# Performance work log

Measured on AMD Instinct MI355X. Metric: run time of the kernel, lower is better.

The kernel has to match this reference:

```python
import jax, jax.numpy as jnp
import numpy as np
from jax import lax

B, T_ENC, T_DEC = 64, 512, 500
MEL, PRE, ENC_D, H, ATT = 80, 256, 512, 1024, 128


def conv1d(x, w, b, pad):
    # x: [B,Cin,T], w: [Cout,Cin,K]
    y = lax.conv_general_dilated(x, w, (1,), [(pad, pad)], dimension_numbers=('NCH', 'OIH', 'NCH'))
    return y + b[None, :, None]


def lstm_cell(x, h, c, w_ih, w_hh, b_ih, b_hh):
    # PyTorch gate order: i, f, g, o
    g = x @ w_ih.T + h @ w_hh.T + b_ih + b_hh
    i, f, gg, o = jnp.split(g, 4, axis=-1)
    c2 = jax.nn.sigmoid(f) * c + jax.nn.sigmoid(i) * jnp.tanh(gg)
    return jax.nn.sigmoid(o) * jnp.tanh(c2), c2


def setup_inputs() -> dict:
    key = jax.random.key(0)
    ks = iter(jax.random.split(key, 64))
    def rn(*shape):
        return jax.random.normal(next(ks), shape, jnp.float32) * 0.05
    return dict(
        enc=jax.random.normal(next(ks), (B, T_ENC, ENC_D), jnp.float32),
        mel_tgt=jax.random.normal(next(ks), (B, T_DEC, MEL), jnp.float32),
        p1w=rn(PRE, MEL), p1b=rn(PRE), p2w=rn(PRE, PRE), p2b=rn(PRE),
        wih0=rn(4 * H, PRE + ENC_D), whh0=rn(4 * H, H), bih0=rn(4 * H), bhh0=rn(4 * H),
        wih1=rn(4 * H, H), whh1=rn(4 * H, H), bih1=rn(4 * H), bhh1=rn(4 * H),
        aq=rn(ATT, H), am=rn(ATT, ENC_D), al=rn(ATT, 32),
        alcw=rn(32, 1, 31), alcb=rn(32), ae=rn(1, ATT), ab=jnp.zeros((ATT,), jnp.float32),
        mw=rn(MEL, H + ENC_D), mb=rn(MEL), sw=rn(1, H + ENC_D), sb=rn(1),
        pw0=rn(512, MEL, 5), pb0=rn(512), bg0=jnp.ones((512,), jnp.float32), bb0=rn(512),
        pw1=rn(512, 512, 5), pb1=rn(512), bg1=jnp.ones((512,), jnp.float32), bb1=rn(512),
        pw2=rn(512, 512, 5), pb2=rn(512), bg2=jnp.ones((512,), jnp.float32), bb2=rn(512),
        pw3=rn(512, 512, 5), pb3=rn(512), bg3=jnp.ones((512,), jnp.float32), bb3=rn(512),
        pw4=rn(MEL, 512, 5), pb4=rn(MEL), bg4=jnp.ones((MEL,), jnp.float32), bb4=rn(MEL),
    )


def reference(enc, mel_tgt, p1w, p1b, p2w, p2b,
              wih0, whh0, bih0, bhh0, wih1, whh1, bih1, bhh1,
              aq, am, al, alcw, alcb, ae, ab, mw, mb, sw, sb,
              pw0, pb0, bg0, bb0, pw1, pb1, bg1, bb1, pw2, pb2, bg2, bb2,
              pw3, pb3, bg3, bb3, pw4, pb4, bg4, bb4):
    Bz, Te, _ = enc.shape
    mem = enc @ am.T  # [B,Te,128] (memory projection hoisted out of the loop)
    # teacher forcing: prev_mel at t=0 is zeros, then mel_tgt[:, t-1]
    prev = jnp.concatenate([jnp.zeros((Bz, 1, MEL), enc.dtype), mel_tgt[:, :-1]], axis=1)
    xs = jnp.swapaxes(prev, 0, 1)  # [Td,B,80]
    init = (jnp.zeros((Bz, Te), enc.dtype),
            jnp.zeros((2, Bz, H), enc.dtype),
            jnp.zeros((2, Bz, H), enc.dtype))

    def step(carry, pm):
        att_prev, h, c = carry
        # prenet (eval mode: dropout disabled)
        pre = jax.nn.relu(jax.nn.relu(pm @ p1w.T + p1b) @ p2w.T + p2b)  # [B,256]
        # location-sensitive attention
        loc = conv1d(att_prev[:, None, :], alcw, alcb, 15)  # [B,32,Te]
        loc = jnp.swapaxes(loc, 1, 2) @ al.T                # [B,Te,128]
        q = (h[1] @ aq.T)[:, None, :]                       # [B,1,128]
        e = jnp.tanh(q + mem + loc + ab) @ ae.T             # [B,Te,1]
        att = jax.nn.softmax(e[..., 0], axis=1)             # [B,Te]
        ctx = jnp.einsum('bt,btd->bd', att, enc)            # [B,512]
        # 2-layer LSTM on single step
        h0, c0 = lstm_cell(jnp.concatenate([pre, ctx], -1), h[0], c[0], wih0, whh0, bih0, bhh0)
        h1, c1 = lstm_cell(h0, h[1], c[1], wih1, whh1, bih1, bhh1)
        pi = jnp.concatenate([h1, ctx], -1)                 # [B,1536]
        mel = pi @ mw.T + mb                                # [B,80]
        stop = pi @ sw.T + sb                               # [B,1]
        return (att, jnp.stack([h0, h1]), jnp.stack([c0, c1])), (mel, stop, att)

    _, (mels, stops, atts) = lax.scan(step, init, xs)
    mel = jnp.swapaxes(mels, 0, 1)    # [B,Td,80]
    stop = jnp.swapaxes(stops, 0, 1)  # [B,Td,1]
    attw = jnp.swapaxes(atts, 0, 1)   # [B,Td,Te]
    # postnet (BatchNorm1d in eval mode: running_mean=0, running_var=1)
    eps = 1e-5
    def bn(x, g, bt):
        return x * (g / jnp.sqrt(1.0 + eps))[None, :, None] + bt[None, :, None]
    x = jnp.swapaxes(mel, 1, 2)  # [B,80,Td]
    x = jnp.tanh(bn(conv1d(x, pw0, pb0, 2), bg0, bb0))
    x = jnp.tanh(bn(conv1d(x, pw1, pb1, 2), bg1, bb1))
    x = jnp.tanh(bn(conv1d(x, pw2, pb2, 2), bg2, bb2))
    x = jnp.tanh(bn(conv1d(x, pw3, pb3, 2), bg3, bb3))
    x = bn(conv1d(x, pw4, pb4, 2), bg4, bb4)
    post = jnp.swapaxes(x, 1, 2)
    return mel + post, mel, stop, attw
```

## Files before the change

### kernel.cpp

```cpp
#include <hip/hip_runtime.h>
#include <math.h>


static constexpr long OFF_AMT  = 0;
static constexpr long OFF_P1WT = OFF_AMT  + 512L*128;
static constexpr long OFF_P2WT = OFF_P1WT + 80L*256;
static constexpr long OFF_MWT  = OFF_P2WT + 256L*256;
static constexpr long OFF_AQT  = OFF_MWT  + 1536L*80;
static constexpr long OFF_WLOC = OFF_AQT  + 1024L*128;
static constexpr long OFF_BLOC = OFF_WLOC + 128L*32;
static constexpr long OFF_WLT  = OFF_BLOC + 128;
static constexpr long OFF_GB0  = OFF_WLT  + 4096;
static constexpr long OFF_GB1  = OFF_GB0  + 4096;
static constexpr long OFF_PWT0 = OFF_GB1  + 4096;
static constexpr long OFF_PWT1 = OFF_PWT0 + 400L*512;
static constexpr long OFF_PWT2 = OFF_PWT1 + 2560L*512;
static constexpr long OFF_PWT3 = OFF_PWT2 + 2560L*512;
static constexpr long OFF_PWT4 = OFF_PWT3 + 2560L*512;
static constexpr long OFF_PRE  = OFF_PWT4 + 2560L*80;
static constexpr long OFF_MEM  = OFF_PRE  + 500L*64*256;
static constexpr long OFF_H0A  = OFF_MEM  + 64L*512*128;
static constexpr long OFF_H0B  = OFF_H0A  + 64L*1024;
static constexpr long OFF_H1A  = OFF_H0B  + 64L*1024;
static constexpr long OFF_H1B  = OFF_H1A  + 64L*1024;
static constexpr long OFF_C0   = OFF_H1B  + 64L*1024;
static constexpr long OFF_C1   = OFF_C0   + 64L*1024;
static constexpr long OFF_Q    = OFF_C1   + 64L*1024;
static constexpr long OFF_CTX  = OFF_Q    + 64L*128;
static constexpr long OFF_EBUF = OFF_CTX  + 64L*512;
static constexpr long OFF_PB0  = OFF_EBUF + 64L*512;
static constexpr long OFF_PB1  = OFF_PB0  + 64L*512*500;
static constexpr long WS_FLOATS = OFF_PB1 + 64L*512*500;

static constexpr long OFF_BAR = OFF_PB0;

static constexpr long DO_MEL  = 64L*500*80;
static constexpr long DO_STOP = 2*DO_MEL;
static constexpr long DO_ATT  = DO_STOP + 64L*500;

static constexpr long ZERO_CNT = OFF_EBUF - OFF_H0A;
static constexpr long PREP_TOTAL = ZERO_CNT + 4096 + 4096 + 4096 + 128 + 4096
  + 65536 + 20480 + 65536 + 122880 + 131072
  + 204800 + 1310720 + 1310720 + 1310720 + 204800;

static constexpr int NBLK = 256;
static constexpr int NTHR = 512;

typedef float f4 __attribute__((ext_vector_type(4)));

__device__ __forceinline__ float fsigmoid(float x) { return 1.f / (1.f + __expf(-x)); }
__device__ __forceinline__ float ftanh(float x) {
  float ax = fminf(fabsf(x), 15.f);
  float e = __expf(-2.f * ax);
  float r = (1.f - e) / (1.f + e);
  return copysignf(r, x);
}
__device__ __forceinline__ float4 ld4(const float* p) { return *(const float4*)p; }
__device__ __forceinline__ f4 ld4v(const float* p) { return *(const f4*)p; }
__device__ __forceinline__ float dot4(float4 w, float4 x, float acc) {
  acc = fmaf(w.x, x.x, acc); acc = fmaf(w.y, x.y, acc);
  acc = fmaf(w.z, x.z, acc); acc = fmaf(w.w, x.w, acc);
  return acc;
}
__device__ __forceinline__ float dot4v(f4 w, float4 x, float acc) {
  acc = fmaf(w.x, x.x, acc); acc = fmaf(w.y, x.y, acc);
  acc = fmaf(w.z, x.z, acc); acc = fmaf(w.w, x.w, acc);
  return acc;
}

__device__ __forceinline__ void gbar(unsigned* bar, unsigned gen) {
  __syncthreads();
  if (blockIdx.x == 0) {
    if (threadIdx.x > 0 && threadIdx.x < 256) {
      while (__hip_atomic_load(&bar[threadIdx.x*16], __ATOMIC_RELAXED,
                               __HIP_MEMORY_SCOPE_AGENT) != gen)
        __builtin_amdgcn_s_sleep(1);
    }
    __syncthreads();
    if (threadIdx.x == 0)
      __hip_atomic_store(&bar[4096], gen, __ATOMIC_RELEASE, __HIP_MEMORY_SCOPE_AGENT);
  } else {
    if (threadIdx.x == 0) {
      __hip_atomic_store(&bar[blockIdx.x*16], gen, __ATOMIC_RELEASE,
                         __HIP_MEMORY_SCOPE_AGENT);
      while (__hip_atomic_load(&bar[4096], __ATOMIC_RELAXED,
                               __HIP_MEMORY_SCOPE_AGENT) != gen)
        __builtin_amdgcn_s_sleep(1);
    }
  }
  if (threadIdx.x == 0) __threadfence();
  __syncthreads();
}

__global__ __launch_bounds__(256) void k_prep(
    const float* __restrict__ bih0, const float* __restrict__ bhh0,
    const float* __restrict__ bih1, const float* __restrict__ bhh1,
    const float* __restrict__ al,   const float* __restrict__ alcw,
    const float* __restrict__ alcb, const float* __restrict__ ab,
    const float* __restrict__ am,   const float* __restrict__ p1w,
    const float* __restrict__ p2w,  const float* __restrict__ mw,
    const float* __restrict__ aq,
    const float* __restrict__ pw0, const float* __restrict__ pw1,
    const float* __restrict__ pw2, const float* __restrict__ pw3,
    const float* __restrict__ pw4,
    float* __restrict__ ws)
{
  if (blockIdx.x == 0) {
    unsigned* bar = (unsigned*)(ws + OFF_BAR);
    for (int i = threadIdx.x; i < 4160; i += 256) bar[i] = 0u;
  }
  long stride = (long)gridDim.x * 256;
  for (long idx = (long)blockIdx.x * 256 + threadIdx.x; idx < PREP_TOTAL; idx += stride) {
    long r = idx;
    if (r < ZERO_CNT) { ws[OFF_H0A + r] = 0.f; continue; }
    r -= ZERO_CNT;
    if (r < 4096) { ws[OFF_GB0 + r] = bih0[r] + bhh0[r]; continue; }
    r -= 4096;
    if (r < 4096) { ws[OFF_GB1 + r] = bih1[r] + bhh1[r]; continue; }
    r -= 4096;
    if (r < 4096) {
      int a = (int)(r >> 5), k = (int)(r & 31);
      float v = 0.f;
      if (k < 31) for (int ch = 0; ch < 32; ++ch) v += al[a*32 + ch] * alcw[ch*31 + k];
      ws[OFF_WLOC + r] = v; continue;
    }
    r -= 4096;
    if (r < 128) {
      float v = ab[r];
      for (int ch = 0; ch < 32; ++ch) v += al[r*32 + ch] * alcb[ch];
      ws[OFF_BLOC + r] = v; continue;
    }
    r -= 128;
    if (r < 4096) {
      int k = (int)(r >> 7), a = (int)(r & 127);
      float v = 0.f;
      if (k < 31) for (int ch = 0; ch < 32; ++ch) v += al[a*32 + ch] * alcw[ch*31 + k];
      ws[OFF_WLT + r] = v; continue;
    }
    r -= 4096;
    if (r < 65536) { int d = (int)(r >> 7), a2 = (int)(r & 127); ws[OFF_AMT + r] = am[(long)a2*512 + d]; continue; }
    r -= 65536;
    if (r < 20480) { int k = (int)(r >> 8), j = (int)(r & 255); ws[OFF_P1WT + r] = p1w[j*80 + k]; continue; }
    r -= 20480;
    if (r < 65536) { int k = (int)(r >> 8), j = (int)(r & 255); ws[OFF_P2WT + r] = p2w[j*256 + k]; continue; }
    r -= 65536;
    if (r < 122880) { int k = (int)(r / 80), c = (int)(r % 80); ws[OFF_MWT + r] = mw[(long)c*1536 + k]; continue; }
    r -= 122880;
    if (r < 131072) { int k = (int)(r >> 7), a2 = (int)(r & 127); ws[OFF_AQT + r] = aq[(long)a2*1024 + k]; continue; }
    r -= 131072;
    if (r < 204800) { int c5 = (int)(r / 512), co = (int)(r % 512); ws[OFF_PWT0 + r] = pw0[((long)co*80  + c5/5)*5 + (c5%5)]; continue; }
    r -= 204800;
    if (r < 1310720) { int c5 = (int)(r / 512), co = (int)(r % 512); ws[OFF_PWT1 + r] = pw1[((long)co*512 + c5/5)*5 + (c5%5)]; continue; }
    r -= 1310720;
    if (r < 1310720) { int c5 = (int)(r / 512), co = (int)(r % 512); ws[OFF_PWT2 + r] = pw2[((long)co*512 + c5/5)*5 + (c5%5)]; continue; }
    r -= 1310720;
    if (r < 1310720) { int c5 = (int)(r / 512), co = (int)(r % 512); ws[OFF_PWT3 + r] = pw3[((long)co*512 + c5/5)*5 + (c5%5)]; continue; }
    r -= 1310720;
    { int c5 = (int)(r / 80), co = (int)(r % 80); ws[OFF_PWT4 + r] = pw4[((long)co*512 + c5/5)*5 + (c5%5)]; }
  }
}

__global__ __launch_bounds__(256) void k_prenet(
    const float* __restrict__ mel_tgt, const float* __restrict__ p1b,
    const float* __restrict__ p2b, float* __restrict__ ws)
{
  int t = blockIdx.x, tid = threadIdx.x;
  const float* p1wT = ws + OFF_P1WT;
  const float* p2wT = ws + OFF_P2WT;
  __shared__ float prev_s[16][80];
  __shared__ float h1_s[16][256];
  for (int sb = 0; sb < 4; ++sb) {
    int b0 = sb * 16;
    for (int i = tid; i < 16*80; i += 256) {
      int rr = i / 80, k = i - rr*80;
      float v = 0.f;
      if (t > 0) v = mel_tgt[((long)(b0 + rr)*500 + (t-1))*80 + k];
      prev_s[rr][k] = v;
    }
    __syncthreads();
    int j = tid;
    for (int rr = 0; rr < 16; ++rr) {
      float acc = p1b[j];
      for (int k = 0; k < 80; ++k) acc = fmaf(prev_s[rr][k], p1wT[k*256 + j], acc);
      h1_s[rr][j] = fmaxf(acc, 0.f);
    }
    __syncthreads();
    for (int rr = 0; rr < 16; ++rr) {
      float acc = p2b[j];
      for (int k = 0; k < 256; ++k) acc = fmaf(h1_s[rr][k], p2wT[k*256 + j], acc);
      ws[OFF_PRE + ((long)t*64 + b0 + rr)*256 + j] = fmaxf(acc, 0.f);
    }
    __syncthreads();
  }
}

__global__ __launch_bounds__(256) void k_mem(const float* __restrict__ enc, float* __restrict__ ws)
{
  int row0 = blockIdx.x * 16;
  int tid = threadIdx.x;
  int a = tid & 127, rh = tid >> 7;
  const float* amT = ws + OFF_AMT;
  __shared__ float encS[16][65];
  float acc[8];
#pragma unroll
  for (int i = 0; i < 8; ++i) acc[i] = 0.f;
  for (int k0 = 0; k0 < 512; k0 += 64) {
    for (int i = tid; i < 16*64; i += 256) {
      int rr = i >> 6, kk = i & 63;
      encS[rr][kk] = enc[(long)(row0 + rr)*512 + k0 + kk];
    }
    __syncthreads();
    for (int kk = 0; kk < 64; ++kk) {
      float w = amT[(long)(k0 + kk)*128 + a];
#pragma unroll
      for (int rr = 0; rr < 8; ++rr) acc[rr] = fmaf(encS[rh*8 + rr][kk], w, acc[rr]);
    }
    __syncthreads();
  }
#pragma unroll
  for (int rr = 0; rr < 8; ++rr)
    ws[OFF_MEM + (long)(row0 + rh*8 + rr)*128 + a] = acc[rr];
}

struct SmemE { float ap[160]; float bq[128]; float ep[4][132]; };
struct SmemS { float es[512]; float wred[8]; float wsum[8]; float red[16][132]; };
struct SmemG { float xw[8][8][64]; float gsh[16][65]; };
struct SmemM { float xs[1536]; };
union SmemU { SmemE e; SmemS s; SmemG g; SmemM m; };

__global__ __launch_bounds__(NTHR, 2) void k_decode(
    const float* __restrict__ enc, const float* __restrict__ ae,
    const float* __restrict__ wih0, const float* __restrict__ whh0,
    const float* __restrict__ wih1, const float* __restrict__ whh1,
    const float* __restrict__ mw, const float* __restrict__ mb,
    const float* __restrict__ sw, const float* __restrict__ sb,
    const float* __restrict__ aq,
    float* __restrict__ dout, float* __restrict__ ws)
{
  const int B = blockIdx.x;
  const int tid = threadIdx.x;
  unsigned* bar = (unsigned*)(ws + OFF_BAR);
  unsigned gen = 0;

  __shared__ float WlTs[4096];
  __shared__ float aeS[128];
  __shared__ SmemU U;

  for (int i = tid; i < 4096; i += NTHR) WlTs[i] = ws[OFF_WLT + i];
  if (tid < 128) aeS[tid] = ae[tid];
  __syncthreads();

  for (int t = 0; t < 500; ++t) {
    const int p = t & 1;

    {
      const int b = B & 63, cc2 = B >> 6;
      const int te0 = cc2 * 128;
      const int tel = tid & 127, ag = tid >> 7;
      const int a0 = ag * 32;
      for (int i = tid; i < 158; i += NTHR) {
        int gte = te0 + i - 15;
        float v = 0.f;
        if (t > 0 && gte >= 0 && gte < 512)
          v = dout[DO_ATT + ((long)b*500 + (t-1))*512 + gte];
        U.e.ap[i] = v;
      }
      if (tid < 128) U.e.bq[tid] = ws[OFF_Q + b*128 + tid] + ws[OFF_BLOC + tid];
      __syncthreads();
      float acc[32];
#pragma unroll
      for (int i = 0; i < 32; ++i) acc[i] = 0.f;
      for (int k = 0; k < 31; ++k) {
        float apk = U.e.ap[tel + k];
#pragma unroll
        for (int a4 = 0; a4 < 8; ++a4) {
          float4 wv = ld4(&WlTs[k*128 + a0 + a4*4]);
          acc[a4*4+0] = fmaf(apk, wv.x, acc[a4*4+0]);
          acc[a4*4+1] = fmaf(apk, wv.y, acc[a4*4+1]);
          acc[a4*4+2] = fmaf(apk, wv.z, acc[a4*4+2]);
          acc[a4*4+3] = fmaf(apk, wv.w, acc[a4*4+3]);
        }
      }
      const float* memp = ws + OFF_MEM + ((long)b*512 + te0 + tel)*128 + a0;
      float esum = 0.f;
#pragma unroll
      for (int a4 = 0; a4 < 8; ++a4) {
        f4 mv = ld4v(&memp[a4*4]);
        float4 bq = ld4(&U.e.bq[a0 + a4*4]);
        float4 av = ld4(&aeS[a0 + a4*4]);
        esum = fmaf(av.x, ftanh(acc[a4*4+0] + bq.x + mv.x), esum);
        esum = fmaf(av.y, ftanh(acc[a4*4+1] + bq.y + mv.y), esum);
        esum = fmaf(av.z, ftanh(acc[a4*4+2] + bq.z + mv.z), esum);
        esum = fmaf(av.w, ftanh(acc[a4*4+3] + bq.w + mv.w), esum);
      }
      U.e.ep[ag][tel] = esum;
      __syncthreads();
      if (tid < 128)
        ws[OFF_EBUF + (long)b*512 + te0 + tid] =
            U.e.ep[0][tid] + U.e.ep[1][tid] + U.e.ep[2][tid] + U.e.ep[3][tid];
    }
    gbar(bar, ++gen);

    {
      const int b = B & 63, q4 = B >> 6;
      const float* eb = ws + OFF_EBUF + (long)b*512;
      float v = eb[tid];
      float m = v;
#pragma unroll
      for (int o = 32; o; o >>= 1) m = fmaxf(m, __shfl_xor(m, o));
      if ((tid & 63) == 0) U.s.wred[tid >> 6] = m;
      __syncthreads();
      float mx = U.s.wred[0];
#pragma unroll
      for (int i2 = 1; i2 < 8; ++i2) mx = fmaxf(mx, U.s.wred[i2]);
      float pe = __expf(v - mx);
      U.s.es[tid] = pe;
      float s = pe;
#pragma unroll
      for (int o = 32; o; o >>= 1) s += __shfl_xor(s, o);
      if ((tid & 63) == 0) U.s.wsum[tid >> 6] = s;
      __syncthreads();
      float tot = U.s.wsum[0];
#pragma unroll
      for (int i2 = 1; i2 < 8; ++i2) tot += U.s.wsum[i2];
      float inv = 1.f / tot;
      if (tid < 128)
        dout[DO_ATT + ((long)b*500 + t)*512 + q4*128 + tid] = U.s.es[q4*128 + tid] * inv;
      const int dq = tid & 31, th = tid >> 5;
      const float* ep = enc + (long)b*262144 + q4*128 + dq*4;
      float4 a4 = {0.f, 0.f, 0.f, 0.f};
#pragma unroll 8
      for (int te = th*32; te < th*32 + 32; ++te) {
        float sc = U.s.es[te];
        f4 ev = ld4v(&ep[(long)te*512]);
        a4.x = fmaf(sc, ev.x, a4.x); a4.y = fmaf(sc, ev.y, a4.y);
        a4.z = fmaf(sc, ev.z, a4.z); a4.w = fmaf(sc, ev.w, a4.w);
      }
      *(float4*)&U.s.red[th][dq*4] = a4;
      __syncthreads();
      if (tid < 128) {
        float sm = 0.f;
#pragma unroll
        for (int th2 = 0; th2 < 16; ++th2) sm += U.s.red[th2][tid];
        ws[OFF_CTX + (long)b*512 + q4*128 + tid] = sm * inv;
      }
    }
    gbar(bar, ++gen);

#pragma unroll 1
    for (int mode = 0; mode < 2; ++mode) {
      const int l = tid & 63, w = tid >> 6;
      const int jr = l & 15, kq = l >> 4;
      const int bs8 = w * 8;
      const long j = (long)(jr >> 2)*1024 + B*4 + (jr & 3);
      const int KH = mode ? 1024 : 768;
      const int LD = mode ? 1024 : 768;
      const int NC = mode ? 32 : 28;
      const float* wih = mode ? wih1 : wih0;
      const float* whh = mode ? whh1 : whh0;
      const float* gbp = ws + (mode ? OFF_GB1 : OFF_GB0);
      const float* srcPre = ws + OFF_PRE + (long)t*64*256;
      const float* srcCtx = ws + OFF_CTX;
      const float* h0r = ws + OFF_H0A + (long)p*65536;
      const float* h0n = ws + OFF_H0A + (long)(1-p)*65536;
      const float* h1r = ws + OFF_H1A + (long)p*65536;
      float* xw = &U.g.xw[w][0][0];

      const int bx0 = l >> 4, kx0 = (l & 15) * 4;

      auto xsrc = [&](int bx, int k) -> float4 {
        const int gb_ = bs8 + bx;
        if (mode == 0) {
          if (k < 256)  return ld4(srcPre + gb_*256 + k);
          if (k < 768)  return ld4(srcCtx + gb_*512 + (k - 256));
          return ld4(h0r + gb_*1024 + (k - 768));
        }
        return (k < 1024) ? ld4(h0n + gb_*1024 + k) : ld4(h1r + gb_*1024 + (k - 1024));
      };

      f4 wr0, wr1, wr2, wr3, wn0, wn1, wn2, wn3;
      float4 xA, xB;
      {
        const int bk = kq * 16;
        const float* wp = (bk < KH) ? (wih + j*LD + bk) : (whh + j*1024 + (bk - KH));
        wr0 = ld4v(wp); wr1 = ld4v(wp + 4); wr2 = ld4v(wp + 8); wr3 = ld4v(wp + 12);
        xA = xsrc(bx0, kx0);
        xB = xsrc(4 + bx0, kx0);
      }
      float acc[8];
#pragma unroll
      for (int i = 0; i < 8; ++i) acc[i] = 0.f;

      for (int c = 0; c < NC; ++c) {
        *(float4*)(xw + l*4)       = xA;
        *(float4*)(xw + 256 + l*4) = xB;
        if (c + 1 < NC) {
          const int bk = (c+1)*64 + kq*16;
          const float* wp = (bk < KH) ? (wih + j*LD + bk) : (whh + j*1024 + (bk - KH));
          wn0 = ld4v(wp); wn1 = ld4v(wp + 4); wn2 = ld4v(wp + 8); wn3 = ld4v(wp + 12);
          xA = xsrc(bx0, (c+1)*64 + kx0);
          xB = xsrc(4 + bx0, (c+1)*64 + kx0);
        }
        asm volatile("s_waitcnt lgkmcnt(0)" ::: "memory");
        __builtin_amdgcn_sched_barrier(0);
#pragma unroll
        for (int i = 0; i < 8; ++i) {
          const float* xp = xw + i*64 + kq*16;
          float4 x0 = ld4(xp), x1 = ld4(xp + 4), x2 = ld4(xp + 8), x3 = ld4(xp + 12);
          acc[i] = dot4v(wr3, x3, dot4v(wr2, x2, dot4v(wr1, x1, dot4v(wr0, x0, acc[i]))));
        }
        __builtin_amdgcn_sched_barrier(0);
        wr0 = wn0; wr1 = wn1; wr2 = wn2; wr3 = wn3;
      }

#pragma unroll
      for (int i = 0; i < 8; ++i) {
        acc[i] += __shfl_xor(acc[i], 16);
        acc[i] += __shfl_xor(acc[i], 32);
      }
      if (kq == 0) {
        float bias = gbp[j];
#pragma unroll
        for (int i = 0; i < 8; ++i) U.g.gsh[jr][bs8 + i] = acc[i] + bias;
      }
      __syncthreads();
      if (tid < 256) {
        const int b2 = tid & 63, u4 = tid >> 6;
        float iv = U.g.gsh[u4][b2];
        float fv = U.g.gsh[4 + u4][b2];
        float gv = U.g.gsh[8 + u4][b2];
        float ov = U.g.gsh[12 + u4][b2];
        long hw = (mode ? OFF_H1A : OFF_H0A) + (long)(1-p)*65536 + (long)b2*1024 + B*4 + u4;
        long cw = (mode ? OFF_C1 : OFF_C0) + (long)b2*1024 + B*4 + u4;
        float cold = ws[cw];
        float c2 = fsigmoid(fv)*cold + fsigmoid(iv)*ftanh(gv);
        ws[cw] = c2;
        ws[hw] = fsigmoid(ov)*ftanh(c2);
      }
      gbar(bar, ++gen);
    }

    {
      const int b = B & 63, part = B >> 6;
      const float* h1n = ws + OFF_H1A + (long)(1-p)*65536;
      const float* ctx = ws + OFF_CTX;
      for (int i = tid; i < 1536; i += NTHR)
        U.m.xs[i] = (i < 1024) ? h1n[b*1024 + i] : ctx[b*512 + (i - 1024)];
      __syncthreads();
      const int grp = tid >> 3, l8 = tid & 7;
      const int kb = l8 * 4;
      if (part == 0 || (part == 3 && grp < 16)) {
        const int jj = (part == 0) ? grp : 64 + grp;
        const float* wrp = mw + (long)jj*1536;
        float4 a4 = {0.f, 0.f, 0.f, 0.f};
#pragma unroll 8
        for (int i = 0; i < 48; ++i) {
          float4 xv = ld4(&U.m.xs[kb + i*32]);
          float4 wv = ld4(&wrp[kb + i*32]);
          a4.x = fmaf(xv.x, wv.x, a4.x); a4.y = fmaf(xv.y, wv.y, a4.y);
          a4.z = fmaf(xv.z, wv.z, a4.z); a4.w = fmaf(xv.w, wv.w, a4.w);
        }
        float acc = (a4.x + a4.y) + (a4.z + a4.w);
        acc += __shfl_xor(acc, 1);
        acc += __shfl_xor(acc, 2);
        acc += __shfl_xor(acc, 4);
        if (l8 == 0) dout[DO_MEL + ((long)b*500 + t)*80 + jj] = acc + mb[jj];
      } else if (part == 1 || part == 2) {
        const int a = (part - 1)*64 + grp;
        const float* wrp = aq + (long)a*1024;
        float4 a4 = {0.f, 0.f, 0.f, 0.f};
#pragma unroll 8
        for (int i = 0; i < 32; ++i) {
          float4 xv = ld4(&U.m.xs[kb + i*32]);
          float4 wv = ld4(&wrp[kb + i*32]);
          a4.x = fmaf(xv.x, wv.x, a4.x); a4.y = fmaf(xv.y, wv.y, a4.y);
          a4.z = fmaf(xv.z, wv.z, a4.z); a4.w = fmaf(xv.w, wv.w, a4.w);
        }
        float acc = (a4.x + a4.y) + (a4.z + a4.w);
        acc += __shfl_xor(acc, 1);
        acc += __shfl_xor(acc, 2);
        acc += __shfl_xor(acc, 4);
        if (l8 == 0) ws[OFF_Q + b*128 + a] = acc;
      } else if (part == 3 && grp == 16) {
        float4 a4 = {0.f, 0.f, 0.f, 0.f};
#pragma unroll 8
        for (int i = 0; i < 48; ++i) {
          float4 xv = ld4(&U.m.xs[kb + i*32]);
          float4 wv = ld4(&sw[kb + i*32]);
          a4.x = fmaf(xv.x, wv.x, a4.x); a4.y = fmaf(xv.y, wv.y, a4.y);
          a4.z = fmaf(xv.z, wv.z, a4.z); a4.w = fmaf(xv.w, wv.w, a4.w);
        }
        float acc = (a4.x + a4.y) + (a4.z + a4.w);
        acc += __shfl_xor(acc, 1);
        acc += __shfl_xor(acc, 2);
        acc += __shfl_xor(acc, 4);
        if (l8 == 0) dout[DO_STOP + (long)b*500 + t] = acc + sb[0];
      }
    }
    gbar(bar, ++gen);
  }
}

__global__ __launch_bounds__(256) void k_conv(
    const float* __restrict__ in, float* __restrict__ out,
    const float* __restrict__ wT, const float* __restrict__ pb,
    const float* __restrict__ bg, const float* __restrict__ bbp,
    const float* __restrict__ melp,
    int CI, int CO, int flags)
{
  int tx = blockIdx.x, cy = blockIdx.y, b = blockIdx.z;
  int tid = threadIdx.x;
  int tl = tid & 63;
  int cog = __builtin_amdgcn_readfirstlane((int)(tid >> 6));
  int t0 = tx * 64;
  int co0 = cy*64 + cog*16;
  __shared__ float xs[16][68];
  float acc[16];
#pragma unroll
  for (int i = 0; i < 16; ++i) acc[i] = 0.f;
  for (int ci0 = 0; ci0 < CI; ci0 += 16) {
    for (int i = tid; i < 16*68; i += 256) {
      int cl = i / 68, tt = i - cl*68;
      int tg = t0 + tt - 2;
      float v = 0.f;
      if (tg >= 0 && tg < 500) {
        if (flags & 1) v = in[((long)b*500 + tg)*80 + (ci0 + cl)];
        else           v = in[((long)b*CI + ci0 + cl)*500 + tg];
      }
      xs[cl][tt] = v;
    }
    __syncthreads();
    for (int cl = 0; cl < 16; ++cl) {
#pragma unroll
      for (int k = 0; k < 5; ++k) {
        const float* wr = wT + ((long)((ci0 + cl)*5 + k))*CO + co0;
        float xv = xs[cl][tl + k];
#pragma unroll
        for (int i = 0; i < 16; ++i) acc[i] = fmaf(xv, wr[i], acc[i]);
      }
    }
    __syncthreads();
  }
  int tg = t0 + tl;
  if (tg < 500) {
    const float RS = 0.99999500003749969f;
#pragma unroll
    for (int i = 0; i < 16; ++i) {
      int co = co0 + i;
      if (co < CO) {
        float sc = bg[co] * RS;
        float v = fmaf(acc[i], sc, fmaf(pb[co], sc, bbp[co]));
        if (flags & 4) v = ftanh(v);
        if (flags & 2) { long oi = ((long)b*500 + tg)*80 + co; out[oi] = melp[oi] + v; }
        else out[((long)b*CO + co)*500 + tg] = v;
      }
    }
  }
}

extern "C" void kernel_launch(void* const* d_in, const int* in_sizes, int n_in,
                              void* d_out, int out_size, void* d_ws, size_t ws_size,
                              hipStream_t stream)
{
  (void)in_sizes; (void)n_in; (void)out_size; (void)ws_size;
  const float* enc     = (const float*)d_in[0];
  const float* mel_tgt = (const float*)d_in[1];
  const float* p1w = (const float*)d_in[2];
  const float* p1b = (const float*)d_in[3];
  const float* p2w = (const float*)d_in[4];
  const float* p2b = (const float*)d_in[5];
  const float* wih0 = (const float*)d_in[6];
  const float* whh0 = (const float*)d_in[7];
  const float* bih0 = (const float*)d_in[8];
  const float* bhh0 = (const float*)d_in[9];
  const float* wih1 = (const float*)d_in[10];
  const float* whh1 = (const float*)d_in[11];
  const float* bih1 = (const float*)d_in[12];
  const float* bhh1 = (const float*)d_in[13];
  const float* aq   = (const float*)d_in[14];
  const float* am   = (const float*)d_in[15];
  const float* al   = (const float*)d_in[16];
  const float* alcw = (const float*)d_in[17];
  const float* alcb = (const float*)d_in[18];
  const float* ae   = (const float*)d_in[19];
  const float* ab   = (const float*)d_in[20];
  const float* mw   = (const float*)d_in[21];
  const float* mb   = (const float*)d_in[22];
  const float* sw   = (const float*)d_in[23];
  const float* sb   = (const float*)d_in[24];
  const float* pw0 = (const float*)d_in[25];
  const float* pb0 = (const float*)d_in[26];
  const float* bg0 = (const float*)d_in[27];
  const float* bb0 = (const float*)d_in[28];
  const float* pw1 = (const float*)d_in[29];
  const float* pb1 = (const float*)d_in[30];
  const float* bg1 = (const float*)d_in[31];
  const float* bb1 = (const float*)d_in[32];
  const float* pw2 = (const float*)d_in[33];
  const float* pb2 = (const float*)d_in[34];
  const float* bg2 = (const float*)d_in[35];
  const float* bb2 = (const float*)d_in[36];
  const float* pw3 = (const float*)d_in[37];
  const float* pb3 = (const float*)d_in[38];
  const float* bg3 = (const float*)d_in[39];
  const float* bb3 = (const float*)d_in[40];
  const float* pw4 = (const float*)d_in[41];
  const float* pb4 = (const float*)d_in[42];
  const float* bg4 = (const float*)d_in[43];
  const float* bb4 = (const float*)d_in[44];

  float* ws = (float*)d_ws;
  float* dout = (float*)d_out;

  k_prep<<<dim3(2048), 256, 0, stream>>>(bih0, bhh0, bih1, bhh1, al, alcw, alcb, ab,
                                         am, p1w, p2w, mw, aq, pw0, pw1, pw2, pw3, pw4, ws);
  k_prenet<<<dim3(500), 256, 0, stream>>>(mel_tgt, p1b, p2b, ws);
  k_mem<<<dim3(2048), 256, 0, stream>>>(enc, ws);

  k_decode<<<dim3(NBLK), NTHR, 0, stream>>>(enc, ae, wih0, whh0, wih1, whh1,
                                            mw, mb, sw, sb, aq, dout, ws);

  k_conv<<<dim3(8, 8, 64), 256, 0, stream>>>(dout + DO_MEL, ws + OFF_PB0, ws + OFF_PWT0,
                                             pb0, bg0, bb0, nullptr, 80, 512, 1 | 4);
  k_conv<<<dim3(8, 8, 64), 256, 0, stream>>>(ws + OFF_PB0, ws + OFF_PB1, ws + OFF_PWT1,
                                             pb1, bg1, bb1, nullptr, 512, 512, 4);
  k_conv<<<dim3(8, 8, 64), 256, 0, stream>>>(ws + OFF_PB1, ws + OFF_PB0, ws + OFF_PWT2,
                                             pb2, bg2, bb2, nullptr, 512, 512, 4);
  k_conv<<<dim3(8, 8, 64), 256, 0, stream>>>(ws + OFF_PB0, ws + OFF_PB1, ws + OFF_PWT3,
                                             pb3, bg3, bb3, nullptr, 512, 512, 4);
  k_conv<<<dim3(8, 2, 64), 256, 0, stream>>>(ws + OFF_PB1, dout, ws + OFF_PWT4,
                                             pb4, bg4, bb4, dout + DO_MEL, 512, 80, 2);
}
```

Before: 95.20 ms.

## Double persistent decode grid to 512 blocks and repartition all per-step phases

The persistent decoder grows from 256 to 512 blocks at 4 blocks per CU. Each block now handles half as much work: 64 encoder positions for the attention energies, 64 context columns, and 2 hidden units per LSTM gate instead of 4, with an extra shuffle stage for the smaller K slices. The grid barrier is extended so block 0 polls 512 arrival flags, and the output-projection phase is reassigned so only the first 256 blocks work. The goal is more parallelism and latency hiding in the weight-streaming GEMV phases, at the cost of a wider barrier and more per-block overhead.

```diff
diff --git a/kernel.cpp b/kernel.cpp
--- a/kernel.cpp
+++ b/kernel.cpp
@@ -43,7 +43,7 @@
   + 65536 + 20480 + 65536 + 122880 + 131072
   + 204800 + 1310720 + 1310720 + 1310720 + 204800;
 
-static constexpr int NBLK = 256;
+static constexpr int NBLK = 512;
 static constexpr int NTHR = 512;
 
 typedef float f4 __attribute__((ext_vector_type(4)));
@@ -57,11 +57,6 @@
 }
 __device__ __forceinline__ float4 ld4(const float* p) { return *(const float4*)p; }
 __device__ __forceinline__ f4 ld4v(const float* p) { return *(const f4*)p; }
-__device__ __forceinline__ float dot4(float4 w, float4 x, float acc) {
-  acc = fmaf(w.x, x.x, acc); acc = fmaf(w.y, x.y, acc);
-  acc = fmaf(w.z, x.z, acc); acc = fmaf(w.w, x.w, acc);
-  return acc;
-}
 __device__ __forceinline__ float dot4v(f4 w, float4 x, float acc) {
   acc = fmaf(w.x, x.x, acc); acc = fmaf(w.y, x.y, acc);
   acc = fmaf(w.z, x.z, acc); acc = fmaf(w.w, x.w, acc);
@@ -71,19 +66,27 @@
 __device__ __forceinline__ void gbar(unsigned* bar, unsigned gen) {
   __syncthreads();
   if (blockIdx.x == 0) {
-    if (threadIdx.x > 0 && threadIdx.x < 256) {
-      while (__hip_atomic_load(&bar[threadIdx.x*16], __ATOMIC_RELAXED,
+    const int t = threadIdx.x;
+    if (t > 0 && t < 256) {
+      while (__hip_atomic_load(&bar[t*16], __ATOMIC_RELAXED,
                                __HIP_MEMORY_SCOPE_AGENT) != gen)
         __builtin_amdgcn_s_sleep(1);
-    }
-    __syncthreads();
-    if (threadIdx.x == 0)
-      __hip_atomic_store(&bar[4096], gen, __ATOMIC_RELEASE, __HIP_MEMORY_SCOPE_AGENT);
+      while (__hip_atomic_load(&bar[(t + 256)*16], __ATOMIC_RELAXED,
+                               __HIP_MEMORY_SCOPE_AGENT) != gen)
+        __builtin_amdgcn_s_sleep(1);
+    } else if (t == 0) {
+      while (__hip_atomic_load(&bar[256*16], __ATOMIC_RELAXED,
+                               __HIP_MEMORY_SCOPE_AGENT) != gen)
+        __builtin_amdgcn_s_sleep(1);
+    }
+    __syncthreads();
+    if (t == 0)
+      __hip_atomic_store(&bar[8192], gen, __ATOMIC_RELEASE, __HIP_MEMORY_SCOPE_AGENT);
   } else {
     if (threadIdx.x == 0) {
       __hip_atomic_store(&bar[blockIdx.x*16], gen, __ATOMIC_RELEASE,
                          __HIP_MEMORY_SCOPE_AGENT);
-      while (__hip_atomic_load(&bar[4096], __ATOMIC_RELAXED,
+      while (__hip_atomic_load(&bar[8192], __ATOMIC_RELAXED,
                                __HIP_MEMORY_SCOPE_AGENT) != gen)
         __builtin_amdgcn_s_sleep(1);
     }
@@ -107,7 +110,7 @@
 {
   if (blockIdx.x == 0) {
     unsigned* bar = (unsigned*)(ws + OFF_BAR);
-    for (int i = threadIdx.x; i < 4160; i += 256) bar[i] = 0u;
+    for (int i = threadIdx.x; i < 8320; i += 256) bar[i] = 0u;
   }
   long stride = (long)gridDim.x * 256;
   for (long idx = (long)blockIdx.x * 256 + threadIdx.x; idx < PREP_TOTAL; idx += stride) {
@@ -222,13 +225,13 @@
     ws[OFF_MEM + (long)(row0 + rh*8 + rr)*128 + a] = acc[rr];
 }
 
-struct SmemE { float ap[160]; float bq[128]; float ep[4][132]; };
-struct SmemS { float es[512]; float wred[8]; float wsum[8]; float red[16][132]; };
-struct SmemG { float xw[8][8][64]; float gsh[16][65]; };
+struct SmemE { float ap[94]; float bq[128]; float ep[8][68]; };
+struct SmemS { float es[512]; float wred[8]; float wsum[8]; float red[32][68]; };
+struct SmemG { float xw[8][8][64]; float gsh[8][65]; };
 struct SmemM { float xs[1536]; };
 union SmemU { SmemE e; SmemS s; SmemG g; SmemM m; };
 
-__global__ __launch_bounds__(NTHR, 2) void k_decode(
+__global__ __launch_bounds__(NTHR, 4) void k_decode(
     const float* __restrict__ enc, const float* __restrict__ ae,
     const float* __restrict__ wih0, const float* __restrict__ whh0,
     const float* __restrict__ wih1, const float* __restrict__ whh1,
@@ -254,26 +257,27 @@
     const int p = t & 1;
 
     {
-      const int b = B & 63, cc2 = B >> 6;
-      const int te0 = cc2 * 128;
-      const int tel = tid & 127, ag = tid >> 7;
-      const int a0 = ag * 32;
-      for (int i = tid; i < 158; i += NTHR) {
-        int gte = te0 + i - 15;
+      const int b = B & 63, cc = B >> 6;
+      const int te0 = cc * 64;
+      const int tel = tid & 63, ag = tid >> 6;
+      const int a0 = ag * 16;
+      if (tid < 94) {
+        int gte = te0 + tid - 15;
         float v = 0.f;
         if (t > 0 && gte >= 0 && gte < 512)
           v = dout[DO_ATT + ((long)b*500 + (t-1))*512 + gte];
-        U.e.ap[i] = v;
-      }
-      if (tid < 128) U.e.bq[tid] = ws[OFF_Q + b*128 + tid] + ws[OFF_BLOC + tid];
+        U.e.ap[tid] = v;
+      }
+      if (tid >= 128 && tid < 256)
+        U.e.bq[tid - 128] = ws[OFF_Q + b*128 + (tid - 128)] + ws[OFF_BLOC + (tid - 128)];
       __syncthreads();
-      float acc[32];
-#pragma unroll
-      for (int i = 0; i < 32; ++i) acc[i] = 0.f;
+      float acc[16];
+#pragma unroll
+      for (int i = 0; i < 16; ++i) acc[i] = 0.f;
       for (int k = 0; k < 31; ++k) {
         float apk = U.e.ap[tel + k];
 #pragma unroll
-        for (int a4 = 0; a4 < 8; ++a4) {
+        for (int a4 = 0; a4 < 4; ++a4) {
           float4 wv = ld4(&WlTs[k*128 + a0 + a4*4]);
           acc[a4*4+0] = fmaf(apk, wv.x, acc[a4*4+0]);
           acc[a4*4+1] = fmaf(apk, wv.y, acc[a4*4+1]);
@@ -284,7 +288,7 @@
       const float* memp = ws + OFF_MEM + ((long)b*512 + te0 + tel)*128 + a0;
       float esum = 0.f;
 #pragma unroll
-      for (int a4 = 0; a4 < 8; ++a4) {
+      for (int a4 = 0; a4 < 4; ++a4) {
         f4 mv = ld4v(&memp[a4*4]);
         float4 bq = ld4(&U.e.bq[a0 + a4*4]);
         float4 av = ld4(&aeS[a0 + a4*4]);
@@ -295,14 +299,18 @@
       }
       U.e.ep[ag][tel] = esum;
       __syncthreads();
-      if (tid < 128)
-        ws[OFF_EBUF + (long)b*512 + te0 + tid] =
-            U.e.ep[0][tid] + U.e.ep[1][tid] + U.e.ep[2][tid] + U.e.ep[3][tid];
+      if (tid < 64) {
+        float s = 0.f;
+#pragma unroll
+        for (int g2 = 0; g2 < 8; ++g2) s += U.e.ep[g2][tid];
+        ws[OFF_EBUF + (long)b*512 + te0 + tid] = s;
+      }
     }
     gbar(bar, ++gen);
 
     {
-      const int b = B & 63, q4 = B >> 6;
+      const int b = B & 63, q8 = B >> 6;
+      const int d0 = q8 * 64;
       const float* eb = ws + OFF_EBUF + (long)b*512;
       float v = eb[tid];
       float m = v;
@@ -324,13 +332,13 @@
 #pragma unroll
       for (int i2 = 1; i2 < 8; ++i2) tot += U.s.wsum[i2];
       float inv = 1.f / tot;
-      if (tid < 128)
-        dout[DO_ATT + ((long)b*500 + t)*512 + q4*128 + tid] = U.s.es[q4*128 + tid] * inv;
-      const int dq = tid & 31, th = tid >> 5;
-      const float* ep = enc + (long)b*262144 + q4*128 + dq*4;
+      if (tid < 64)
+        dout[DO_ATT + ((long)b*500 + t)*512 + d0 + tid] = U.s.es[d0 + tid] * inv;
+      const int dq = tid & 15, th = tid >> 4;
+      const float* ep = enc + (long)b*262144 + d0 + dq*4;
       float4 a4 = {0.f, 0.f, 0.f, 0.f};
 #pragma unroll 8
-      for (int te = th*32; te < th*32 + 32; ++te) {
+      for (int te = th*16; te < th*16 + 16; ++te) {
         float sc = U.s.es[te];
         f4 ev = ld4v(&ep[(long)te*512]);
         a4.x = fmaf(sc, ev.x, a4.x); a4.y = fmaf(sc, ev.y, a4.y);
@@ -338,11 +346,11 @@
       }
       *(float4*)&U.s.red[th][dq*4] = a4;
       __syncthreads();
-      if (tid < 128) {
+      if (tid < 64) {
         float sm = 0.f;
 #pragma unroll
-        for (int th2 = 0; th2 < 16; ++th2) sm += U.s.red[th2][tid];
-        ws[OFF_CTX + (long)b*512 + q4*128 + tid] = sm * inv;
+        for (int th2 = 0; th2 < 32; ++th2) sm += U.s.red[th2][tid];
+        ws[OFF_CTX + (long)b*512 + d0 + tid] = sm * inv;
       }
     }
     gbar(bar, ++gen);
@@ -350,9 +358,9 @@
 #pragma unroll 1
     for (int mode = 0; mode < 2; ++mode) {
       const int l = tid & 63, w = tid >> 6;
-      const int jr = l & 15, kq = l >> 4;
+      const int jr = l & 7, kq = l >> 3;
       const int bs8 = w * 8;
-      const long j = (long)(jr >> 2)*1024 + B*4 + (jr & 3);
+      const long j = (long)(jr >> 1)*1024 + B*2 + (jr & 1);
       const int KH = mode ? 1024 : 768;
       const int LD = mode ? 1024 : 768;
       const int NC = mode ? 32 : 28;
@@ -366,10 +374,10 @@
       const float* h1r = ws + OFF_H1A + (long)p*65536;
       float* xw = &U.g.xw[w][0][0];
 
-      const int bx0 = l >> 4, kx0 = (l & 15) * 4;
-
-      auto xsrc = [&](int bx, int k) -> float4 {
-        const int gb_ = bs8 + bx;
+      const int bx0 = l >> 3, kx0 = (l & 7) * 8;
+
+      auto xsrc = [&](int k) -> float4 {
+        const int gb_ = bs8 + bx0;
         if (mode == 0) {
           if (k < 256)  return ld4(srcPre + gb_*256 + k);
           if (k < 768)  return ld4(srcCtx + gb_*512 + (k - 256));
@@ -378,43 +386,44 @@
         return (k < 1024) ? ld4(h0n + gb_*1024 + k) : ld4(h1r + gb_*1024 + (k - 1024));
       };
 
-      f4 wr0, wr1, wr2, wr3, wn0, wn1, wn2, wn3;
+      f4 wr0, wr1, wn0, wn1;
       float4 xA, xB;
       {
-        const int bk = kq * 16;
+        const int bk = kq * 8;
         const float* wp = (bk < KH) ? (wih + j*LD + bk) : (whh + j*1024 + (bk - KH));
-        wr0 = ld4v(wp); wr1 = ld4v(wp + 4); wr2 = ld4v(wp + 8); wr3 = ld4v(wp + 12);
-        xA = xsrc(bx0, kx0);
-        xB = xsrc(4 + bx0, kx0);
+        wr0 = ld4v(wp); wr1 = ld4v(wp + 4);
+        xA = xsrc(kx0);
+        xB = xsrc(kx0 + 4);
       }
       float acc[8];
 #pragma unroll
       for (int i = 0; i < 8; ++i) acc[i] = 0.f;
 
       for (int c = 0; c < NC; ++c) {
-        *(float4*)(xw + l*4)       = xA;
-        *(float4*)(xw + 256 + l*4) = xB;
+        *(float4*)(xw + l*8)     = xA;
+        *(float4*)(xw + l*8 + 4) = xB;
         if (c + 1 < NC) {
-          const int bk = (c+1)*64 + kq*16;
+          const int bk = (c+1)*64 + kq*8;
           const float* wp = (bk < KH) ? (wih + j*LD + bk) : (whh + j*1024 + (bk - KH));
-          wn0 = ld4v(wp); wn1 = ld4v(wp + 4); wn2 = ld4v(wp + 8); wn3 = ld4v(wp + 12);
-          xA = xsrc(bx0, (c+1)*64 + kx0);
-          xB = xsrc(4 + bx0, (c+1)*64 + kx0);
+          wn0 = ld4v(wp); wn1 = ld4v(wp + 4);
+          xA = xsrc((c+1)*64 + kx0);
+          xB = xsrc((c+1)*64 + kx0 + 4);
         }
         asm volatile("s_waitcnt lgkmcnt(0)" ::: "memory");
         __builtin_amdgcn_sched_barrier(0);
 #pragma unroll
         for (int i = 0; i < 8; ++i) {
-          const float* xp = xw + i*64 + kq*16;
-          float4 x0 = ld4(xp), x1 = ld4(xp + 4), x2 = ld4(xp + 8), x3 = ld4(xp + 12);
-          acc[i] = dot4v(wr3, x3, dot4v(wr2, x2, dot4v(wr1, x1, dot4v(wr0, x0, acc[i]))));
+          const float* xp = xw + i*64 + kq*8;
+          float4 x0 = ld4(xp), x1 = ld4(xp + 4);
+          acc[i] = dot4v(wr1, x1, dot4v(wr0, x0, acc[i]));
         }
         __builtin_amdgcn_sched_barrier(0);
-        wr0 = wn0; wr1 = wn1; wr2 = wn2; wr3 = wn3;
+        wr0 = wn0; wr1 = wn1;
       }
 
 #pragma unroll
       for (int i = 0; i < 8; ++i) {
+        acc[i] += __shfl_xor(acc[i], 8);
         acc[i] += __shfl_xor(acc[i], 16);
         acc[i] += __shfl_xor(acc[i], 32);
       }
@@ -424,14 +433,14 @@
         for (int i = 0; i < 8; ++i) U.g.gsh[jr][bs8 + i] = acc[i] + bias;
       }
       __syncthreads();
-      if (tid < 256) {
-        const int b2 = tid & 63, u4 = tid >> 6;
-        float iv = U.g.gsh[u4][b2];
-        float fv = U.g.gsh[4 + u4][b2];
-        float gv = U.g.gsh[8 + u4][b2];
-        float ov = U.g.gsh[12 + u4][b2];
-        long hw = (mode ? OFF_H1A : OFF_H0A) + (long)(1-p)*65536 + (long)b2*1024 + B*4 + u4;
-        long cw = (mode ? OFF_C1 : OFF_C0) + (long)b2*1024 + B*4 + u4;
+      if (tid < 128) {
+        const int b2 = tid & 63, u2 = tid >> 6;
+        float iv = U.g.gsh[u2][b2];
+        float fv = U.g.gsh[2 + u2][b2];
+        float gv = U.g.gsh[4 + u2][b2];
+        float ov = U.g.gsh[6 + u2][b2];
+        long hw = (mode ? OFF_H1A : OFF_H0A) + (long)(1-p)*65536 + (long)b2*1024 + B*2 + u2;
+        long cw = (mode ? OFF_C1 : OFF_C0) + (long)b2*1024 + B*2 + u2;
         float cold = ws[cw];
         float c2 = fsigmoid(fv)*cold + fsigmoid(iv)*ftanh(gv);
         ws[cw] = c2;
@@ -442,59 +451,61 @@
 
     {
       const int b = B & 63, part = B >> 6;
-      const float* h1n = ws + OFF_H1A + (long)(1-p)*65536;
-      const float* ctx = ws + OFF_CTX;
-      for (int i = tid; i < 1536; i += NTHR)
-        U.m.xs[i] = (i < 1024) ? h1n[b*1024 + i] : ctx[b*512 + (i - 1024)];
-      __syncthreads();
-      const int grp = tid >> 3, l8 = tid & 7;
-      const int kb = l8 * 4;
-      if (part == 0 || (part == 3 && grp < 16)) {
-        const int jj = (part == 0) ? grp : 64 + grp;
-        const float* wrp = mw + (long)jj*1536;
-        float4 a4 = {0.f, 0.f, 0.f, 0.f};
+      if (part < 4) {
+        const float* h1n = ws + OFF_H1A + (long)(1-p)*65536;
+        const float* ctx = ws + OFF_CTX;
+        for (int i = tid; i < 1536; i += NTHR)
+          U.m.xs[i] = (i < 1024) ? h1n[b*1024 + i] : ctx[b*512 + (i - 1024)];
+        __syncthreads();
+        const int grp = tid >> 3, l8 = tid & 7;
+        const int kb = l8 * 4;
+        if (part == 0 || (part == 1 && grp < 16)) {
+          const int jj = (part == 0) ? grp : 64 + grp;
+          const float* wrp = mw + (long)jj*1536;
+          float4 a4 = {0.f, 0.f, 0.f, 0.f};
 #pragma unroll 8
-        for (int i = 0; i < 48; ++i) {
-          float4 xv = ld4(&U.m.xs[kb + i*32]);
-          float4 wv = ld4(&wrp[kb + i*32]);
-          a4.x = fmaf(xv.x, wv.x, a4.x); a4.y = fmaf(xv.y, wv.y, a4.y);
-          a4.z = fmaf(xv.z, wv.z, a4.z); a4.w = fmaf(xv.w, wv.w, a4.w);
+          for (int i = 0; i < 48; ++i) {
+            float4 xv = ld4(&U.m.xs[kb + i*32]);
+            float4 wv = ld4(&wrp[kb + i*32]);
+            a4.x = fmaf(xv.x, wv.x, a4.x); a4.y = fmaf(xv.y, wv.y, a4.y);
+            a4.z = fmaf(xv.z, wv.z, a4.z); a4.w = fmaf(xv.w, wv.w, a4.w);
+          }
+          float acc = (a4.x + a4.y) + (a4.z + a4.w);
+          acc += __shfl_xor(acc, 1);
+          acc += __shfl_xor(acc, 2);
+          acc += __shfl_xor(acc, 4);
+          if (l8 == 0) dout[DO_MEL + ((long)b*500 + t)*80 + jj] = acc + mb[jj];
+        } else if (part == 1 && grp == 16) {
+          float4 a4 = {0.f, 0.f, 0.f, 0.f};
+#pragma unroll 8
+          for (int i = 0; i < 48; ++i) {
+            float4 xv = ld4(&U.m.xs[kb + i*32]);
+            float4 wv = ld4(&sw[kb + i*32]);
+            a4.x = fmaf(xv.x, wv.x, a4.x); a4.y = fmaf(xv.y, wv.y, a4.y);
+            a4.z = fmaf(xv.z, wv.z, a4.z); a4.w = fmaf(xv.w, wv.w, a4.w);
+          }
+          float acc = (a4.x + a4.y) + (a4.z + a4.w);
+          acc += __shfl_xor(acc, 1);
+          acc += __shfl_xor(acc, 2);
+          acc += __shfl_xor(acc, 4);
+          if (l8 == 0) dout[DO_STOP + (long)b*500 + t] = acc + sb[0];
+        } else if (part >= 2) {
+          const int a = (part - 2)*64 + grp;
+          const float* wrp = aq + (long)a*1024;
+          float4 a4 = {0.f, 0.f, 0.f, 0.f};
+#pragma unroll 8
+          for (int i = 0; i < 32; ++i) {
+            float4 xv = ld4(&U.m.xs[kb + i*32]);
+            float4 wv = ld4(&wrp[kb + i*32]);
+            a4.x = fmaf(xv.x, wv.x, a4.x); a4.y = fmaf(xv.y, wv.y, a4.y);
+            a4.z = fmaf(xv.z, wv.z, a4.z); a4.w = fmaf(xv.w, wv.w, a4.w);
+          }
+          float acc = (a4.x + a4.y) + (a4.z + a4.w);
+          acc += __shfl_xor(acc, 1);
+          acc += __shfl_xor(acc, 2);
+          acc += __shfl_xor(acc, 4);
+          if (l8 == 0) ws[OFF_Q + b*128 + a] = acc;
         }
-        float acc = (a4.x + a4.y) + (a4.z + a4.w);
-        acc += __shfl_xor(acc, 1);
-        acc += __shfl_xor(acc, 2);
-        acc += __shfl_xor(acc, 4);
-        if (l8 == 0) dout[DO_MEL + ((long)b*500 + t)*80 + jj] = acc + mb[jj];
-      } else if (part == 1 || part == 2) {
-        const int a = (part - 1)*64 + grp;
-        const float* wrp = aq + (long)a*1024;
-        float4 a4 = {0.f, 0.f, 0.f, 0.f};
-#pragma unroll 8
-        for (int i = 0; i < 32; ++i) {
-          float4 xv = ld4(&U.m.xs[kb + i*32]);
-          float4 wv = ld4(&wrp[kb + i*32]);
-          a4.x = fmaf(xv.x, wv.x, a4.x); a4.y = fmaf(xv.y, wv.y, a4.y);
-          a4.z = fmaf(xv.z, wv.z, a4.z); a4.w = fmaf(xv.w, wv.w, a4.w);
-        }
-        float acc = (a4.x + a4.y) + (a4.z + a4.w);
-        acc += __shfl_xor(acc, 1);
-        acc += __shfl_xor(acc, 2);
-        acc += __shfl_xor(acc, 4);
-        if (l8 == 0) ws[OFF_Q + b*128 + a] = acc;
-      } else if (part == 3 && grp == 16) {
-        float4 a4 = {0.f, 0.f, 0.f, 0.f};
-#pragma unroll 8
-        for (int i = 0; i < 48; ++i) {
-          float4 xv = ld4(&U.m.xs[kb + i*32]);
-          float4 wv = ld4(&sw[kb + i*32]);
-          a4.x = fmaf(xv.x, wv.x, a4.x); a4.y = fmaf(xv.y, wv.y, a4.y);
-          a4.z = fmaf(xv.z, wv.z, a4.z); a4.w = fmaf(xv.w, wv.w, a4.w);
-        }
-        float acc = (a4.x + a4.y) + (a4.z + a4.w);
-        acc += __shfl_xor(acc, 1);
-        acc += __shfl_xor(acc, 2);
-        acc += __shfl_xor(acc, 4);
-        if (l8 == 0) dout[DO_STOP + (long)b*500 + t] = acc + sb[0];
       }
     }
     gbar(bar, ++gen);
```

Result: slower. 198.8 ms (+108.9%).
